# Optimization experiments

Hardware: AMD Instinct MI355X
Metric: run time of the kernel (lower is better)

Reference implementation:

```python
import jax, jax.numpy as jnp
import numpy as np

N = 100000          # nodes
E = 1600000         # edges per adjacency (avg degree 16)
DIMS = [256, 128, 64]
ALPHA = 0.8
WD = 1e-4


def setup_inputs() -> dict:
    key = jax.random.key(0)
    ks = jax.random.split(key, 11)
    X = jax.random.normal(ks[0], (N, DIMS[0]), jnp.float32)
    rows = jax.random.randint(ks[1], (E,), 0, N, jnp.int32)
    cols = jax.random.randint(ks[2], (E,), 0, N, jnp.int32)
    prune_rows = jax.random.randint(ks[3], (E,), 0, N, jnp.int32)
    prune_cols = jax.random.randint(ks[4], (E,), 0, N, jnp.int32)
    # learned params (torch.randn init, scaled 0.1 for fp32 numeric headroom)
    W0 = jax.random.normal(ks[5], (DIMS[0], DIMS[1]), jnp.float32) * 0.1
    W1 = jax.random.normal(ks[6], (DIMS[1], DIMS[2]), jnp.float32) * 0.1
    v00 = jax.random.normal(ks[7], (DIMS[1], 1), jnp.float32) * 0.1
    v01 = jax.random.normal(ks[8], (DIMS[1], 1), jnp.float32) * 0.1
    pv00 = jax.random.normal(ks[9], (DIMS[1], 1), jnp.float32) * 0.1
    pv01 = jax.random.normal(ks[10], (DIMS[1], 1), jnp.float32) * 0.1
    return {"X": X, "W0": W0, "W1": W1, "v00": v00, "v01": v01,
            "pv00": pv00, "pv01": pv01, "rows": rows, "cols": cols,
            "prune_rows": prune_rows, "prune_cols": prune_cols}


def _edge_softmax(rows, logits, n):
    # row-wise softmax over sparse edge logits
    m = jax.ops.segment_max(logits, rows, num_segments=n)
    e = jnp.exp(logits - m[rows])
    s = jax.ops.segment_sum(e, rows, num_segments=n)
    return e / s[rows]


def _attention(rows, cols, H, va, vb, n):
    # logit_e = (H @ va)[src_e] + (H @ vb)[dst_e]  (binary adjacency values)
    f1 = (H @ va)[:, 0]
    f2 = (H @ vb)[:, 0]
    return _edge_softmax(rows, f1[rows] + f2[cols], n)


def _spmm(rows, cols, vals, H, n):
    # out[i] = sum_{e: rows[e]==i} vals[e] * H[cols[e]]
    return jax.ops.segment_sum(vals[:, None] * H[cols], rows, num_segments=n)


def reference(X, W0, W1, v00, v01, pv00, pv01, rows, cols, prune_rows, prune_cols):
    n = X.shape[0]
    # ---- encoder ----
    H1 = X @ W0                                   # layer 0 projection
    c = _attention(rows, cols, H1, v00, v01, n)   # C[0]
    pc = _attention(prune_rows, prune_cols, H1, pv00, pv01, n)  # prune_C[0]
    H1a = (1.0 - ALPHA) * _spmm(rows, cols, c, H1, n) \
        + ALPHA * _spmm(prune_rows, prune_cols, pc, H1, n)
    H1a = jax.nn.elu(H1a)                         # nonlinear, layer 0 != last
    H_enc = H1a @ W1                              # layer 1 == last: no attention
    # ---- decoder ----
    D = H_enc @ W1.T                              # layer 1
    D = (1.0 - ALPHA) * _spmm(rows, cols, c, D, n) \
        + ALPHA * _spmm(prune_rows, prune_cols, pc, D, n)
    D = jax.nn.elu(D)                             # nonlinear, layer 1 != 0
    X_ = D @ W0.T                                 # layer 0: plain matmul
    # ---- loss ----
    loss = jnp.sqrt(jnp.sum((X - X_) ** 2)) \
         + WD * (jnp.sum(W0 ** 2) + jnp.sum(W1 ** 2))
    return (loss, H_enc, X_)
```

## Files before the change

kernel.cpp:

```cpp
#include <hip/hip_runtime.h>
#include <math.h>

#define N_NODES 100000
#define N_EDGES 1600000
#define TOT (2 * N_NODES)
#define SCAN_NB 256
#define SCAN_CH 4

static inline int cdiv(long a, long b) { return (int)((a + b - 1) / b); }

typedef unsigned int uint;
typedef unsigned short ushort;
typedef __attribute__((ext_vector_type(8))) short short8v;
typedef __attribute__((ext_vector_type(4))) float f32x4;

__device__ inline float bf2f(uint u) { return __uint_as_float(u << 16); }
__device__ inline ushort f2bf(float f) {
    uint u = __float_as_uint(f);
    uint r = ((u >> 16) & 1u) + 0x7fffu;
    return (ushort)((u + r) >> 16);
}

template <int K, int M, bool AF32, int OUT, bool ELU, bool LOSS, bool ATTN>
__global__ __launch_bounds__(256) void gemm_mfma(const void* __restrict__ Av,
                                                 const ushort* __restrict__ Bcm,
                                                 void* __restrict__ Cv,
                                                 void* __restrict__ Cv2,
                                                 const float* __restrict__ Xref,
                                                 float* __restrict__ partial,
                                                 const float* __restrict__ va,
                                                 const float* __restrict__ vb,
                                                 const float* __restrict__ pva,
                                                 const float* __restrict__ pvb,
                                                 float* __restrict__ f1,
                                                 float* __restrict__ f2,
                                                 float* __restrict__ pf1,
                                                 float* __restrict__ pf2,
                                                 int nrows) {
    constexpr int BM = 128;
    constexpr int KP = K + 8;
    constexpr int NCT = M / 16;
    __shared__ ushort Blds[M * KP];
    __shared__ ushort Alds[BM * 32];
    const int w = threadIdx.x >> 6;
    const int l = threadIdx.x & 63;
    const int rowg = l & 15;
    const int kg = l >> 4;
    const int rbase = blockIdx.x * BM;
    {
        const uint4* src = reinterpret_cast<const uint4*>(Bcm);
        uint4* dst = reinterpret_cast<uint4*>(Blds);
        const int total = M * KP / 8;
        for (int i = threadIdx.x; i < total; i += 256) dst[i] = src[i];
    }
    f32x4 acc[2][NCT] = {};
    for (int k0 = 0; k0 < K; k0 += 32) {
        __syncthreads();
        int r = threadIdx.x >> 1;
        int kk = (threadIdx.x & 1) * 16;
        int rg = min(rbase + r, nrows - 1);
        if (AF32) {
            const float* A = (const float*)Av;
            const float4* src = reinterpret_cast<const float4*>(A + (size_t)rg * K + k0 + kk);
            ushort* dst = &Alds[r * 32 + kk];
#pragma unroll
            for (int q = 0; q < 4; ++q) {
                float4 v = src[q];
                dst[4 * q + 0] = f2bf(v.x); dst[4 * q + 1] = f2bf(v.y);
                dst[4 * q + 2] = f2bf(v.z); dst[4 * q + 3] = f2bf(v.w);
            }
        } else {
            const ushort* A = (const ushort*)Av;
            const uint4* src = reinterpret_cast<const uint4*>(A + (size_t)rg * K + k0 + kk);
            uint4* dst = reinterpret_cast<uint4*>(&Alds[r * 32 + kk]);
            dst[0] = src[0];
            dst[1] = src[1];
        }
        __syncthreads();
#pragma unroll
        for (int rt = 0; rt < 2; ++rt) {
            short8v af = *reinterpret_cast<const short8v*>(
                &Alds[(w * 32 + rt * 16 + rowg) * 32 + kg * 8]);
#pragma unroll
            for (int ct = 0; ct < NCT; ++ct) {
                short8v bf = *reinterpret_cast<const short8v*>(
                    &Blds[(ct * 16 + rowg) * KP + k0 + kg * 8]);
                acc[rt][ct] = __builtin_amdgcn_mfma_f32_16x16x32_bf16(
                    af, bf, acc[rt][ct], 0, 0, 0);
            }
        }
    }
    float lsum = 0.f;
#pragma unroll
    for (int rt = 0; rt < 2; ++rt) {
#pragma unroll
        for (int q = 0; q < 4; ++q) {
            int r = rbase + w * 32 + rt * 16 + kg * 4 + q;
            if (r >= nrows) continue;
#pragma unroll
            for (int ct = 0; ct < NCT; ++ct) {
                float o = acc[rt][ct][q];
                if (ELU) o = o > 0.f ? o : expm1f(o);
                int col = ct * 16 + rowg;
                if (OUT == 0 || OUT == 3) ((float*)Cv)[(size_t)r * M + col] = o;
                if (OUT == 2) ((ushort*)Cv)[(size_t)r * M + col] = f2bf(o);
                if (OUT == 3) ((ushort*)Cv2)[(size_t)r * M + col] = f2bf(o);
                if (LOSS) {
                    float d = o - Xref[(size_t)r * 256 + col];
                    lsum += d * d;
                }
            }
        }
    }
    if (ATTN) {
        float var[NCT], vbr[NCT], pvar[NCT], pvbr[NCT];
#pragma unroll
        for (int ct = 0; ct < NCT; ++ct) {
            int col = ct * 16 + rowg;
            var[ct] = va[col]; vbr[ct] = vb[col];
            pvar[ct] = pva[col]; pvbr[ct] = pvb[col];
        }
#pragma unroll
        for (int rt = 0; rt < 2; ++rt) {
#pragma unroll
            for (int q = 0; q < 4; ++q) {
                int r = rbase + w * 32 + rt * 16 + kg * 4 + q;
                float da = 0.f, db = 0.f, dpa = 0.f, dpb = 0.f;
#pragma unroll
                for (int ct = 0; ct < NCT; ++ct) {
                    float o = acc[rt][ct][q];
                    da += o * var[ct]; db += o * vbr[ct];
                    dpa += o * pvar[ct]; dpb += o * pvbr[ct];
                }
#pragma unroll
                for (int m = 1; m < 16; m <<= 1) {
                    da += __shfl_xor(da, m); db += __shfl_xor(db, m);
                    dpa += __shfl_xor(dpa, m); dpb += __shfl_xor(dpb, m);
                }
                if (rowg == 0 && r < nrows) {
                    f1[r] = da; f2[r] = db; pf1[r] = dpa; pf2[r] = dpb;
                }
            }
        }
    }
    if (LOSS) {
        __shared__ float smRed[4];
#pragma unroll
        for (int off = 32; off > 0; off >>= 1) lsum += __shfl_down(lsum, off);
        __syncthreads();
        if (l == 0) smRed[w] = lsum;
        __syncthreads();
        if (threadIdx.x == 0)
            partial[blockIdx.x] = smRed[0] + smRed[1] + smRed[2] + smRed[3];
    }
}

__global__ __launch_bounds__(256) void prep_all_kernel(const float* __restrict__ W0,
                                                       ushort* __restrict__ B1,
                                                       ushort* __restrict__ B8) {
    int i = blockIdx.x * 256 + threadIdx.x;
    if (i < 32768) {
        int k = i / 128, m = i - k * 128;
        B1[m * 264 + k] = f2bf(W0[i]);
    } else if (i < 65536) {
        int j = i - 32768;
        int m = j / 128, k = j - m * 128;
        B8[m * 136 + k] = f2bf(W0[j]);
    }
}

__global__ __launch_bounds__(256) void hist2_kernel(const int* __restrict__ rows,
                                                    const int* __restrict__ prows,
                                                    int* __restrict__ deg) {
    int e = blockIdx.x * 256 + threadIdx.x;
    if (e >= 2 * N_EDGES) return;
    int b = e < N_EDGES ? rows[e] * 2 : prows[e - N_EDGES] * 2 + 1;
    atomicAdd(&deg[b], 1);
}

__device__ inline int pad8(int d) { return (d + 7) & ~7; }

__global__ __launch_bounds__(256) void scan1_kernel(const int* __restrict__ deg,
                                                    int* __restrict__ bsum) {
    __shared__ int sm[256];
    int base = (blockIdx.x * 256 + threadIdx.x) * SCAN_CH;
    int s = 0;
#pragma unroll
    for (int i = 0; i < SCAN_CH; ++i) {
        int idx = base + i;
        if (idx < TOT) s += pad8(deg[idx]);
    }
    sm[threadIdx.x] = s;
    __syncthreads();
    for (int off = 128; off > 0; off >>= 1) {
        if (threadIdx.x < off) sm[threadIdx.x] += sm[threadIdx.x + off];
        __syncthreads();
    }
    if (threadIdx.x == 0) bsum[blockIdx.x] = sm[0];
}

__global__ __launch_bounds__(256) void scan3_kernel(const int* __restrict__ deg,
                                                    const int* __restrict__ bsum,
                                                    int* __restrict__ rp) {
    __shared__ int sm[256];
    __shared__ int base0;
    if (threadIdx.x == 0) {
        int run = 0;
        for (int i = 0; i < blockIdx.x; ++i) run += bsum[i];
        base0 = run;
    }
    int base = (blockIdx.x * 256 + threadIdx.x) * SCAN_CH;
    int s = 0;
#pragma unroll
    for (int i = 0; i < SCAN_CH; ++i) {
        int idx = base + i;
        if (idx < TOT) s += pad8(deg[idx]);
    }
    sm[threadIdx.x] = s;
    __syncthreads();
    if (threadIdx.x == 0) {
        int run = base0;
        for (int t = 0; t < 256; ++t) { int tmp = sm[t]; sm[t] = run; run += tmp; }
    }
    __syncthreads();
    int off = sm[threadIdx.x];
#pragma unroll
    for (int i = 0; i < SCAN_CH; ++i) {
        int idx = base + i;
        if (idx < TOT) { rp[idx] = off; off += pad8(deg[idx]); }
        else if (idx == TOT) rp[idx] = off;
    }
}

__global__ __launch_bounds__(256) void scatter_kernel(const int* __restrict__ rlist,
                                                      const int* __restrict__ clist,
                                                      int adj,
                                                      const int* __restrict__ rp,
                                                      int* __restrict__ cur,
                                                      int* __restrict__ ccol) {
    int e = blockIdx.x * 256 + threadIdx.x;
    if (e >= N_EDGES) return;
    int b = rlist[e] * 2 + adj;
    int pos = rp[b] + atomicAdd(&cur[b], 1);
    ccol[pos] = clist[e];
}

__global__ __launch_bounds__(256) void edgeval_kernel(const int* __restrict__ rp,
                                                      const int* __restrict__ deg,
                                                      const int* __restrict__ ccol,
                                                      const float* __restrict__ f1,
                                                      const float* __restrict__ f2,
                                                      const float* __restrict__ pf1,
                                                      const float* __restrict__ pf2,
                                                      int2* __restrict__ eg) {
    int b = blockIdx.x * 16 + (threadIdx.x >> 4);
    int sl = threadIdx.x & 15;
    int adj = b & 1, r = b >> 1;
    float f1r = adj ? pf1[r] : f1[r];
    const float* f2t = adj ? pf2 : f2;
    float scale = adj ? 0.8f : 0.2f;
    int j0 = rp[b];
    int realend = j0 + deg[b];
    int pend = rp[b + 1];
    float s = 0.f;
    for (int j = j0 + sl; j < realend; j += 16)
        s += __expf(f1r + f2t[ccol[j]]);
#pragma unroll
    for (int off = 8; off > 0; off >>= 1) s += __shfl_xor(s, off);
    float inv = s > 0.f ? scale / s : 0.f;
    for (int j = j0 + sl; j < pend; j += 16) {
        if (j < realend) {
            int c = ccol[j];
            float wv = __expf(f1r + f2t[c]) * inv;
            eg[j] = make_int2(c, __float_as_int(wv));
        } else {
            eg[j] = make_int2(0, 0);
        }
    }
}

#define SPU 8
__global__ __launch_bounds__(256) void spmm_enc_kernel(const int* __restrict__ rp,
                                                       const int2* __restrict__ eg,
                                                       const ushort* __restrict__ Hb,
                                                       const float* __restrict__ W1,
                                                       float* __restrict__ Henc,
                                                       ushort* __restrict__ HencB) {
    __shared__ ushort W1lds[128 * 72];
    __shared__ float sRow[4][128];
    for (int i = threadIdx.x; i < 8192; i += 256) {
        int k = i >> 6, m = i & 63;
        W1lds[k * 72 + m] = f2bf(W1[i]);
    }
    __syncthreads();
    int r = blockIdx.x * 4 + (threadIdx.x >> 6);
    int wid = threadIdx.x >> 6;
    int lane = threadIdx.x & 63;
    const uint* Hu = reinterpret_cast<const uint*>(Hb);
    float a0 = 0.f, a1 = 0.f;
    int j = rp[2 * r], E = rp[2 * r + 2];
    if (j < E) {
        int2 d[SPU]; uint h[SPU];
#pragma unroll
        for (int u = 0; u < SPU; ++u) d[u] = eg[j + u];
#pragma unroll
        for (int u = 0; u < SPU; ++u) h[u] = Hu[(uint)d[u].x * 64u + lane];
        j += SPU;
        for (; j < E; j += SPU) {
            int2 dn[SPU]; uint hn[SPU];
#pragma unroll
            for (int u = 0; u < SPU; ++u) dn[u] = eg[j + u];
#pragma unroll
            for (int u = 0; u < SPU; ++u) hn[u] = Hu[(uint)dn[u].x * 64u + lane];
#pragma unroll
            for (int u = 0; u < SPU; ++u) {
                float v = __int_as_float(d[u].y);
                a0 += v * bf2f(h[u] & 0xffffu);
                a1 += v * bf2f(h[u] >> 16);
            }
#pragma unroll
            for (int u = 0; u < SPU; ++u) { d[u] = dn[u]; h[u] = hn[u]; }
        }
#pragma unroll
        for (int u = 0; u < SPU; ++u) {
            float v = __int_as_float(d[u].y);
            a0 += v * bf2f(h[u] & 0xffffu);
            a1 += v * bf2f(h[u] >> 16);
        }
    }
    a0 = a0 > 0.f ? a0 : expm1f(a0);
    a1 = a1 > 0.f ? a1 : expm1f(a1);
    sRow[wid][2 * lane] = a0;
    sRow[wid][2 * lane + 1] = a1;
    asm volatile("s_waitcnt lgkmcnt(0)" ::: "memory");
    __builtin_amdgcn_sched_barrier(0);
    float acc = 0.f;
#pragma unroll 8
    for (int k = 0; k < 128; ++k)
        acc += sRow[wid][k] * bf2f((uint)W1lds[k * 72 + lane]);
    Henc[(size_t)r * 64 + lane] = acc;
    HencB[(size_t)r * 64 + lane] = f2bf(acc);
}

__global__ __launch_bounds__(256) void spmm_dec_kernel(const int* __restrict__ rp,
                                                       const int2* __restrict__ eg,
                                                       const ushort* __restrict__ Hb,
                                                       const float* __restrict__ W1,
                                                       uint* __restrict__ Dh) {
    __shared__ ushort WTlds[64 * 136];
    __shared__ float sRow[4][64];
    for (int i = threadIdx.x; i < 8192; i += 256) {
        int m = i >> 6, k = i & 63;
        WTlds[k * 136 + m] = f2bf(W1[i]);
    }
    __syncthreads();
    int r = blockIdx.x * 4 + (threadIdx.x >> 6);
    int wid = threadIdx.x >> 6;
    int lane = threadIdx.x & 63;
    float a = 0.f;
    int j = rp[2 * r], E = rp[2 * r + 2];
    if (j < E) {
        int2 d[SPU]; ushort h[SPU];
#pragma unroll
        for (int u = 0; u < SPU; ++u) d[u] = eg[j + u];
#pragma unroll
        for (int u = 0; u < SPU; ++u) h[u] = Hb[(uint)d[u].x * 64u + lane];
        j += SPU;
        for (; j < E; j += SPU) {
            int2 dn[SPU]; ushort hn[SPU];
#pragma unroll
            for (int u = 0; u < SPU; ++u) dn[u] = eg[j + u];
#pragma unroll
            for (int u = 0; u < SPU; ++u) hn[u] = Hb[(uint)dn[u].x * 64u + lane];
#pragma unroll
            for (int u = 0; u < SPU; ++u)
                a += __int_as_float(d[u].y) * bf2f((uint)h[u]);
#pragma unroll
            for (int u = 0; u < SPU; ++u) { d[u] = dn[u]; h[u] = hn[u]; }
        }
#pragma unroll
        for (int u = 0; u < SPU; ++u)
            a += __int_as_float(d[u].y) * bf2f((uint)h[u]);
    }
    sRow[wid][lane] = a;
    asm volatile("s_waitcnt lgkmcnt(0)" ::: "memory");
    __builtin_amdgcn_sched_barrier(0);
    float d0 = 0.f, d1 = 0.f;
#pragma unroll 8
    for (int k = 0; k < 64; ++k) {
        float sv = sRow[wid][k];
        uint wv = *reinterpret_cast<const uint*>(&WTlds[k * 136 + 2 * lane]);
        d0 += sv * bf2f(wv & 0xffffu);
        d1 += sv * bf2f(wv >> 16);
    }
    d0 = d0 > 0.f ? d0 : expm1f(d0);
    d1 = d1 > 0.f ? d1 : expm1f(d1);
    Dh[(size_t)r * 64 + lane] = (uint)f2bf(d0) | ((uint)f2bf(d1) << 16);
}

__global__ __launch_bounds__(256) void sqw_reduce_kernel(const float* __restrict__ W0,
                                                         const float* __restrict__ W1,
                                                         float* __restrict__ acc) {
    __shared__ float sm[4];
    float s = 0.f;
    for (int i = blockIdx.x * 256 + threadIdx.x; i < 40960; i += gridDim.x * 256) {
        float d = i < 32768 ? W0[i] : W1[i - 32768];
        s += d * d;
    }
#pragma unroll
    for (int off = 32; off > 0; off >>= 1) s += __shfl_down(s, off);
    int lane = threadIdx.x & 63, w = threadIdx.x >> 6;
    if (lane == 0) sm[w] = s;
    __syncthreads();
    if (threadIdx.x == 0) atomicAdd(acc, sm[0] + sm[1] + sm[2] + sm[3]);
}

__global__ __launch_bounds__(256) void partial_reduce_kernel(const float* __restrict__ p,
                                                             int n, float* __restrict__ acc) {
    __shared__ float sm[4];
    float s = 0.f;
    for (int i = threadIdx.x; i < n; i += 256) s += p[i];
#pragma unroll
    for (int off = 32; off > 0; off >>= 1) s += __shfl_down(s, off);
    int lane = threadIdx.x & 63, w = threadIdx.x >> 6;
    if (lane == 0) sm[w] = s;
    __syncthreads();
    if (threadIdx.x == 0) atomicAdd(acc, sm[0] + sm[1] + sm[2] + sm[3]);
}

__global__ void finalize_kernel(const float* __restrict__ acc, float* __restrict__ out) {
    out[0] = sqrtf(acc[0]) + 1e-4f * acc[1];
}

extern "C" void kernel_launch(void* const* d_in, const int* in_sizes, int n_in,
                              void* d_out, int out_size, void* d_ws, size_t ws_size,
                              hipStream_t stream) {
    const float* X    = (const float*)d_in[0];
    const float* W0   = (const float*)d_in[1];
    const float* W1   = (const float*)d_in[2];
    const float* v00  = (const float*)d_in[3];
    const float* v01  = (const float*)d_in[4];
    const float* pv00 = (const float*)d_in[5];
    const float* pv01 = (const float*)d_in[6];
    const int* rows   = (const int*)d_in[7];
    const int* cols   = (const int*)d_in[8];
    const int* prows  = (const int*)d_in[9];
    const int* pcols  = (const int*)d_in[10];

    float* out  = (float*)d_out;
    float* Henc = out + 1;
    float* Xrec = out + 1 + (size_t)N_NODES * 64;

    ushort* bufAh  = (ushort*)(out + 6400004);
    int*    ccol   = (int*)(out + 12800004);
    int2*   eg     = (int2*)(out + 17600004);
    ushort* HencB  = (ushort*)(out + 27200004);
    int*    deg    = (int*)(out + 28800004);
    int*    cur    = deg + TOT;

    float* ws   = (float*)d_ws;
    ushort* bufBh = (ushort*)ws;
    float* f1   = ws + (size_t)N_NODES * 128;
    float* f2   = f1 + N_NODES;
    float* pf1  = f2 + N_NODES;
    float* pf2  = pf1 + N_NODES;
    float* acc  = pf2 + N_NODES;
    ushort* B1cm = (ushort*)(acc + 4);
    ushort* B8cm = B1cm + 128 * 264;
    int*   rp   = (int*)(B8cm + 256 * 136);
    int*   bsum = rp + TOT + 1;
    float* partial = (float*)(bsum + SCAN_NB);

    const int n = N_NODES;
    const int EG = cdiv(N_EDGES, 256);
    const int EG2 = cdiv(2 * (long)N_EDGES, 256);

    prep_all_kernel<<<cdiv(65536, 256), 256, 0, stream>>>(W0, B1cm, B8cm);

    gemm_mfma<256, 128, true, 2, false, false, true><<<cdiv(n, 128), 256, 0, stream>>>(
        X, B1cm, bufAh, nullptr, nullptr, nullptr,
        v00, v01, pv00, pv01, f1, f2, pf1, pf2, n);

    hipMemsetAsync(deg, 0, 2 * (size_t)TOT * sizeof(int), stream);
    hipMemsetAsync(acc, 0, 4 * sizeof(float), stream);

    hist2_kernel<<<EG2, 256, 0, stream>>>(rows, prows, deg);
    scan1_kernel<<<SCAN_NB, 256, 0, stream>>>(deg, bsum);
    scan3_kernel<<<SCAN_NB, 256, 0, stream>>>(deg, bsum, rp);
    scatter_kernel<<<EG, 256, 0, stream>>>(rows, cols, 0, rp, cur, ccol);
    scatter_kernel<<<EG, 256, 0, stream>>>(prows, pcols, 1, rp, cur, ccol);
    edgeval_kernel<<<cdiv(TOT, 16), 256, 0, stream>>>(rp, deg, ccol,
                                                      f1, f2, pf1, pf2, eg);

    spmm_enc_kernel<<<n / 4, 256, 0, stream>>>(rp, eg, bufAh, W1, Henc, HencB);

    spmm_dec_kernel<<<n / 4, 256, 0, stream>>>(rp, eg, HencB, W1, (uint*)bufBh);

    gemm_mfma<128, 256, false, 0, false, true, false><<<cdiv(n, 128), 256, 0, stream>>>(
        bufBh, B8cm, Xrec, nullptr, X, partial,
        nullptr, nullptr, nullptr, nullptr, nullptr, nullptr, nullptr, nullptr, n);

    partial_reduce_kernel<<<1, 256, 0, stream>>>(partial, cdiv(n, 128), acc + 0);
    sqw_reduce_kernel<<<20, 256, 0, stream>>>(W0, W1, acc + 1);
    finalize_kernel<<<1, 1, 0, stream>>>(acc, out);
}
```

Baseline: 763.1 us.

## Split decoder spmm from W1^T projection and run projection on MFMA GEMM

The decoder kernel previously did the 64-wide sparse aggregation and then a scalar per-row 64x128 projection with ELU through LDS. It now writes the aggregated rows as bf16 to a scratch buffer and runs the W1^T projection plus ELU in the existing MFMA GEMM template. The W1 bf16 column-major layout is prepared once in prep_all instead of per block. This adds an extra kernel launch and a write/read round trip of an N x 64 bf16 intermediate. In exchange it removes the scalar FMA loop and the per-block LDS transpose of W1.

```diff
diff --git a/kernel.cpp b/kernel.cpp
--- a/kernel.cpp
+++ b/kernel.cpp
@@ -156,7 +156,9 @@
 }
 
 __global__ __launch_bounds__(256) void prep_all_kernel(const float* __restrict__ W0,
+                                                       const float* __restrict__ W1,
                                                        ushort* __restrict__ B1,
+                                                       ushort* __restrict__ B7,
                                                        ushort* __restrict__ B8) {
     int i = blockIdx.x * 256 + threadIdx.x;
     if (i < 32768) {
@@ -166,6 +168,10 @@
         int j = i - 32768;
         int m = j / 128, k = j - m * 128;
         B8[m * 136 + k] = f2bf(W0[j]);
+    } else if (i < 73728) {
+        int j = i - 65536;
+        int m = j / 64, k = j - m * 64;
+        B7[m * 72 + k] = f2bf(W1[j]);
     }
 }
 
@@ -342,20 +348,11 @@
     HencB[(size_t)r * 64 + lane] = f2bf(acc);
 }
 
-__global__ __launch_bounds__(256) void spmm_dec_kernel(const int* __restrict__ rp,
-                                                       const int2* __restrict__ eg,
-                                                       const ushort* __restrict__ Hb,
-                                                       const float* __restrict__ W1,
-                                                       uint* __restrict__ Dh) {
-    __shared__ ushort WTlds[64 * 136];
-    __shared__ float sRow[4][64];
-    for (int i = threadIdx.x; i < 8192; i += 256) {
-        int m = i >> 6, k = i & 63;
-        WTlds[k * 136 + m] = f2bf(W1[i]);
-    }
-    __syncthreads();
+__global__ __launch_bounds__(256) void spmm64_fused_kernel(const int* __restrict__ rp,
+                                                           const int2* __restrict__ eg,
+                                                           const ushort* __restrict__ Hb,
+                                                           ushort* __restrict__ Sh) {
     int r = blockIdx.x * 4 + (threadIdx.x >> 6);
-    int wid = threadIdx.x >> 6;
     int lane = threadIdx.x & 63;
     float a = 0.f;
     int j = rp[2 * r], E = rp[2 * r + 2];
@@ -382,20 +379,7 @@
         for (int u = 0; u < SPU; ++u)
             a += __int_as_float(d[u].y) * bf2f((uint)h[u]);
     }
-    sRow[wid][lane] = a;
-    asm volatile("s_waitcnt lgkmcnt(0)" ::: "memory");
-    __builtin_amdgcn_sched_barrier(0);
-    float d0 = 0.f, d1 = 0.f;
-#pragma unroll 8
-    for (int k = 0; k < 64; ++k) {
-        float sv = sRow[wid][k];
-        uint wv = *reinterpret_cast<const uint*>(&WTlds[k * 136 + 2 * lane]);
-        d0 += sv * bf2f(wv & 0xffffu);
-        d1 += sv * bf2f(wv >> 16);
-    }
-    d0 = d0 > 0.f ? d0 : expm1f(d0);
-    d1 = d1 > 0.f ? d1 : expm1f(d1);
-    Dh[(size_t)r * 64 + lane] = (uint)f2bf(d0) | ((uint)f2bf(d1) << 16);
+    Sh[(size_t)r * 64 + lane] = f2bf(a);
 }
 
 __global__ __launch_bounds__(256) void sqw_reduce_kernel(const float* __restrict__ W0,
@@ -452,6 +436,7 @@
     float* Xrec = out + 1 + (size_t)N_NODES * 64;
 
     ushort* bufAh  = (ushort*)(out + 6400004);
+    ushort* Sh     = (ushort*)(out + 6400004);
     int*    ccol   = (int*)(out + 12800004);
     int2*   eg     = (int2*)(out + 17600004);
     ushort* HencB  = (ushort*)(out + 27200004);
@@ -466,7 +451,8 @@
     float* pf2  = pf1 + N_NODES;
     float* acc  = pf2 + N_NODES;
     ushort* B1cm = (ushort*)(acc + 4);
-    ushort* B8cm = B1cm + 128 * 264;
+    ushort* B7cm = B1cm + 128 * 264;
+    ushort* B8cm = B7cm + 128 * 72;
     int*   rp   = (int*)(B8cm + 256 * 136);
     int*   bsum = rp + TOT + 1;
     float* partial = (float*)(bsum + SCAN_NB);
@@ -475,7 +461,7 @@
     const int EG = cdiv(N_EDGES, 256);
     const int EG2 = cdiv(2 * (long)N_EDGES, 256);
 
-    prep_all_kernel<<<cdiv(65536, 256), 256, 0, stream>>>(W0, B1cm, B8cm);
+    prep_all_kernel<<<cdiv(73728, 256), 256, 0, stream>>>(W0, W1, B1cm, B7cm, B8cm);
 
     gemm_mfma<256, 128, true, 2, false, false, true><<<cdiv(n, 128), 256, 0, stream>>>(
         X, B1cm, bufAh, nullptr, nullptr, nullptr,
@@ -494,7 +480,11 @@
 
     spmm_enc_kernel<<<n / 4, 256, 0, stream>>>(rp, eg, bufAh, W1, Henc, HencB);
 
-    spmm_dec_kernel<<<n / 4, 256, 0, stream>>>(rp, eg, HencB, W1, (uint*)bufBh);
+    spmm64_fused_kernel<<<n / 4, 256, 0, stream>>>(rp, eg, HencB, Sh);
+
+    gemm_mfma<64, 128, false, 2, true, false, false><<<cdiv(n, 128), 256, 0, stream>>>(
+        Sh, B7cm, bufBh, nullptr, nullptr, nullptr,
+        nullptr, nullptr, nullptr, nullptr, nullptr, nullptr, nullptr, nullptr, n);
 
     gemm_mfma<128, 256, false, 0, false, true, false><<<cdiv(n, 128), 256, 0, stream>>>(
         bufBh, B8cm, Xrec, nullptr, X, partial,
```

Measured after the change: 762.3 us. Within noise of the previous version (-0.1%).
